# Kernel optimization log

Hardware: AMD Instinct MI355X
Metric: run time of the kernel (lower is better)

The kernel has to match this reference:

```python
import jax, jax.numpy as jnp
import numpy as np

SLOPE = 0.01  # torch LeakyReLU default negative_slope

def lrelu(x):
    return jax.nn.leaky_relu(x, SLOPE)

def rgcn_conv(x, edge_index, edge_type, rel_w, root_w, bias, num_relations=2):
    # PyG RGCNConv: out = x @ root + bias + sum_r mean_{edges of rel r into i}(x_j @ W_r)
    N = x.shape[0]
    src, dst = edge_index[0], edge_index[1]
    out = x @ root_w + bias
    # transform once per relation at node level, then gather per edge
    h = jnp.einsum('nd,rde->rne', x, rel_w)          # [R, N, d]
    msg = h[edge_type, src]                           # [E, d] single gather
    for r in range(num_relations):
        m = (edge_type == r)
        s = jax.ops.segment_sum(jnp.where(m[:, None], msg, 0.0), dst, num_segments=N)
        cnt = jax.ops.segment_sum(m.astype(x.dtype), dst, num_segments=N)
        out = out + s / jnp.maximum(cnt, 1.0)[:, None]  # mean aggregation (0 if no edges)
    return out


def setup_inputs() -> dict:
    key = jax.random.key(0)
    ks = jax.random.split(key, 24)
    N, E, H = 50000, 800000, 256
    Q = H // 4
    def lin(k, i, o):
        k1, k2 = jax.random.split(k)
        s = 1.0 / np.sqrt(i)
        return (jax.random.uniform(k1, (i, o), jnp.float32, -s, s),
                jax.random.uniform(k2, (o,), jnp.float32, -s, s))
    Wd, bd = lin(ks[0], 768, Q)
    Wt, bt = lin(ks[1], 768, Q)
    Wn, bn = lin(ks[2], 5, Q)
    Wc, bc = lin(ks[3], 3, Q)
    Wi, bi = lin(ks[4], H, H)
    Wo1, bo1 = lin(ks[5], H, H)
    Wo2, bo2 = lin(ks[6], H, 2)
    s = 1.0 / np.sqrt(H)
    rel_w1 = jax.random.uniform(ks[7], (2, H, H), jnp.float32, -s, s)
    root_w1 = jax.random.uniform(ks[8], (H, H), jnp.float32, -s, s)
    bias1 = jnp.zeros((H,), jnp.float32)
    rel_w2 = jax.random.uniform(ks[9], (2, H, H), jnp.float32, -s, s)
    root_w2 = jax.random.uniform(ks[10], (H, H), jnp.float32, -s, s)
    bias2 = jnp.zeros((H,), jnp.float32)
    return {
        'des': jax.random.normal(ks[11], (N, 768), jnp.float32),
        'tweet': jax.random.normal(ks[12], (N, 768), jnp.float32),
        'num_prop': jax.random.normal(ks[13], (N, 5), jnp.float32),
        'cat_prop': jax.random.normal(ks[14], (N, 3), jnp.float32),
        'edge_index': jax.random.randint(ks[15], (2, E), 0, N, jnp.int32),
        'edge_type': jax.random.randint(ks[16], (E,), 0, 2, jnp.int32),
        'Wd': Wd, 'bd': bd, 'Wt': Wt, 'bt': bt, 'Wn': Wn, 'bn': bn, 'Wc': Wc, 'bc': bc,
        'Wi': Wi, 'bi': bi,
        'rel_w1': rel_w1, 'root_w1': root_w1, 'bias1': bias1,
        'rel_w2': rel_w2, 'root_w2': root_w2, 'bias2': bias2,
        'Wo1': Wo1, 'bo1': bo1, 'Wo2': Wo2, 'bo2': bo2,
    }


def reference(des, tweet, num_prop, cat_prop, edge_index, edge_type,
              Wd, bd, Wt, bt, Wn, bn, Wc, bc, Wi, bi,
              rel_w1, root_w1, bias1, rel_w2, root_w2, bias2,
              Wo1, bo1, Wo2, bo2):
    # dropout is identity in eval mode
    d = lrelu(des @ Wd + bd)
    t = lrelu(tweet @ Wt + bt)
    n = lrelu(num_prop @ Wn + bn)
    c = lrelu(cat_prop @ Wc + bc)
    x = jnp.concatenate([d, t, n, c], axis=1)           # [N, H]
    x = lrelu(x @ Wi + bi)
    x = rgcn_conv(x, edge_index, edge_type, rel_w1, root_w1, bias1)
    x = rgcn_conv(x, edge_index, edge_type, rel_w2, root_w2, bias2)
    x = lrelu(x @ Wo1 + bo1)
    return x @ Wo2 + bo2                                 # [N, 2]
```

## Files before the change

kernel.cpp:

```cpp
#include <hip/hip_runtime.h>
#include <stdint.h>

__device__ __forceinline__ float bf2f(unsigned short h) {
    union { unsigned int u; float f; } x;
    x.u = ((unsigned int)h) << 16;
    return x.f;
}
__device__ __forceinline__ unsigned short f2bf(float f) {
    union { float f; unsigned int u; } x;
    x.f = f;
    unsigned int u = x.u;
    unsigned int r = (u + 0x7FFFu + ((u >> 16) & 1u)) >> 16;
    return (unsigned short)r;
}
__device__ __forceinline__ float ldf(const void* p, size_t i, int f32) {
    return f32 ? ((const float*)p)[i] : bf2f(((const unsigned short*)p)[i]);
}

typedef __attribute__((ext_vector_type(8))) short short8;
typedef __attribute__((ext_vector_type(4))) float floatx4;

__global__ void k_detect(const unsigned short* __restrict__ p, int* flag) {
    __shared__ int cnt;
    if (threadIdx.x == 0) cnt = 0;
    __syncthreads();
    int c = 0;
    for (int i = threadIdx.x; i < 4096; i += 256) {
        unsigned e = (p[i] >> 7) & 0xFFu;
        if (e >= 0xC0u) c++;
    }
    atomicAdd(&cnt, c);
    __syncthreads();
    if (threadIdx.x == 0) *flag = (cnt > 32) ? 1 : 0;
}

template <int BN, bool TWO>
__global__ __launch_bounds__(256) void gemm_nt(
    const void* __restrict__ A0, const void* __restrict__ A1,
    const void* __restrict__ A2, int o0, int o1, int o2, int lda,
    const unsigned short* __restrict__ Bt, int ldb,
    unsigned short* __restrict__ C, int ldc,
    const unsigned short* __restrict__ bias,
    int M, int K, int act, const int* __restrict__ dflag,
    const void* Ab = nullptr, const unsigned short* Btb = nullptr,
    unsigned short* Cb = nullptr, const unsigned short* biasb = nullptr)
{
    constexpr int BM = 128, BK = 64;
    constexpr int NJ = (BN == 128) ? 4 : 2;
    const int af32 = dflag ? *dflag : 0;
    const int tid  = threadIdx.x;
    const int wave = tid >> 6;
    const int lane = tid & 63;
    const int quad = lane >> 4;
    const int l16  = lane & 15;
    const int m0   = blockIdx.x * BM;
    const int wm   = (wave & 1) * 64;
    const int wn   = (wave >> 1) * (BN / 2);
    int n0;
    const unsigned short* BtS;
    unsigned short* CS;
    const unsigned short* biasS;
    const void *A0S, *A1S, *A2S;
    if (TWO && blockIdx.y == 1) {
        n0 = 0; BtS = Btb; CS = Cb; biasS = biasb;
        A0S = Ab; A1S = Ab; A2S = Ab;
    } else {
        n0 = TWO ? 0 : blockIdx.y * BN;
        BtS = Bt; CS = C; biasS = bias;
        A0S = A0; A1S = A1; A2S = A2;
    }

    __shared__ short8 As[8 * (BM + 2)];
    __shared__ short8 Bs[8 * (BN + 2)];

    floatx4 acc[4][NJ];
#pragma unroll
    for (int i = 0; i < 4; i++)
#pragma unroll
        for (int j = 0; j < NJ; j++) acc[i][j] = (floatx4){0.f, 0.f, 0.f, 0.f};

    for (int kt = 0; kt < K; kt += BK) {
        const void* Ap = (kt < 256) ? A0S : (kt < 512) ? A1S : A2S;
        const int Ao = (kt < 256) ? o0 : (kt < 512) ? o1 : o2;
        const int ko = kt & 255;
#pragma unroll
        for (int c = 0; c < 4; c++) {
            int lin = c * 256 + tid;
            int row = lin >> 3, kq = lin & 7;
            int gr = m0 + row; if (gr > M - 1) gr = M - 1;
            size_t eoff = (size_t)gr * lda + Ao + ko + kq * 8;
            short8 v;
            if (af32) {
                const float4* pf = (const float4*)((const float*)Ap + eoff);
                float4 f0 = pf[0];
                float4 f1 = pf[1];
                v[0] = (short)f2bf(f0.x); v[1] = (short)f2bf(f0.y);
                v[2] = (short)f2bf(f0.z); v[3] = (short)f2bf(f0.w);
                v[4] = (short)f2bf(f1.x); v[5] = (short)f2bf(f1.y);
                v[6] = (short)f2bf(f1.z); v[7] = (short)f2bf(f1.w);
            } else {
                v = *(const short8*)((const unsigned short*)Ap + eoff);
            }
            As[kq * (BM + 2) + row] = v;
        }
#pragma unroll
        for (int c = 0; c < (BN * 8) / 256; c++) {
            int lin = c * 256 + tid;
            int n = lin >> 3, kq = lin & 7;
            short8 v = *(const short8*)(BtS + (size_t)(n0 + n) * ldb + kt + kq * 8);
            Bs[kq * (BN + 2) + n] = v;
        }
        __syncthreads();
#pragma unroll
        for (int s = 0; s < 2; s++) {
            short8 af[4], bfr[NJ];
#pragma unroll
            for (int i = 0; i < 4; i++)
                af[i] = As[(s * 4 + quad) * (BM + 2) + wm + i * 16 + l16];
#pragma unroll
            for (int j = 0; j < NJ; j++)
                bfr[j] = Bs[(s * 4 + quad) * (BN + 2) + wn + j * 16 + l16];
#pragma unroll
            for (int i = 0; i < 4; i++)
#pragma unroll
                for (int j = 0; j < NJ; j++)
                    acc[i][j] = __builtin_amdgcn_mfma_f32_16x16x32_bf16(
                        af[i], bfr[j], acc[i][j], 0, 0, 0);
        }
        __syncthreads();
    }

#pragma unroll
    for (int j = 0; j < NJ; j++) {
        int gc = n0 + wn + j * 16 + l16;
        float bv = biasS ? bf2f(biasS[gc]) : 0.f;
#pragma unroll
        for (int i = 0; i < 4; i++) {
            int grb = m0 + wm + i * 16 + quad * 4;
#pragma unroll
            for (int r = 0; r < 4; r++) {
                int gr = grb + r;
                if (gr < M) {
                    float v = acc[i][j][r] + bv;
                    if (act) v = v > 0.f ? v : 0.01f * v;
                    CS[(size_t)gr * ldc + gc] = f2bf(v);
                }
            }
        }
    }
}

__global__ void t_cvt(const void* __restrict__ in, unsigned short* __restrict__ out,
                      int R, int C, const int* __restrict__ dflag) {
    int f32 = *dflag;
    int i = blockIdx.x * 256 + threadIdx.x;
    if (i < R * C) {
        int r = i / C, c = i % C;
        out[(size_t)c * R + r] = f2bf(ldf(in, i, f32));
    }
}

__global__ void build_bt(const void* __restrict__ root, const void* __restrict__ rel,
                         unsigned short* __restrict__ out, int H,
                         const int* __restrict__ dflag) {
    int f32 = *dflag;
    int i = blockIdx.x * 256 + threadIdx.x;
    int K3 = 3 * H;
    if (i < H * K3) {
        int k = i % K3;
        int n = i / K3;
        float v = (k < H) ? ldf(root, (size_t)k * H + n, f32)
                          : ldf(rel, (size_t)(k - H) * H + n, f32);
        out[i] = f2bf(v);
    }
}

__global__ void k_biases(const void* bd, const void* bt, const void* bi,
                         const void* b1, const void* b2, const void* bo1,
                         unsigned short* __restrict__ out, const int* __restrict__ dflag) {
    int f32 = *dflag;
    for (int idx = threadIdx.x; idx < 1152; idx += 256) {
        const void* p; int off;
        if (idx < 64)       { p = bd;  off = idx; }
        else if (idx < 128) { p = bt;  off = idx - 64; }
        else if (idx < 384) { p = bi;  off = idx - 128; }
        else if (idx < 640) { p = b1;  off = idx - 384; }
        else if (idx < 896) { p = b2;  off = idx - 640; }
        else                { p = bo1; off = idx - 896; }
        out[idx] = f2bf(ldf(p, off, f32));
    }
}

__global__ void k_hist(const int* __restrict__ ei, const int* __restrict__ et,
                       int* cnt2, int N, int E) {
    int e = blockIdx.x * 256 + threadIdx.x;
    if (e < E) {
        int dst = ei[E + e];
        int t = et[e] & 1;
        if ((unsigned)dst < (unsigned)N) atomicAdd(&cnt2[t * N + dst], 1);
    }
}

__global__ void k_scan1(const int* __restrict__ cnt2, int* rowptr, int* bsum, int N) {
    __shared__ int sh[256];
    int t = threadIdx.x;
    int base = blockIdx.x * 1024 + t * 4;
    int v[4];
    int s = 0;
#pragma unroll
    for (int k = 0; k < 4; k++) {
        int idx = base + k;
        v[k] = (idx < N) ? (cnt2[idx] + cnt2[N + idx]) : 0;
        s += v[k];
    }
    sh[t] = s;
    __syncthreads();
    for (int off = 1; off < 256; off <<= 1) {
        int x = 0;
        if (t >= off) x = sh[t - off];
        __syncthreads();
        if (t >= off) sh[t] += x;
        __syncthreads();
    }
    int excl = sh[t] - s;
    int run = excl;
#pragma unroll
    for (int k = 0; k < 4; k++) {
        int idx = base + k;
        if (idx < N) rowptr[idx] = run;
        run += v[k];
    }
    if (t == 255) bsum[blockIdx.x] = sh[255];
}

__global__ void k_scan2(const int* __restrict__ bsum, int* bofs, int nb) {
    int t = threadIdx.x;
    int v = (t < nb) ? bsum[t] : 0;
    int orig = v;
    for (int off = 1; off < 64; off <<= 1) {
        int x = __shfl_up(v, off);
        if (t >= off) v += x;
    }
    if (t < nb) bofs[t] = v - orig;
}

__global__ void k_scan3(int* rowptr, const int* __restrict__ bofs, int N) {
    int i = blockIdx.x * 256 + threadIdx.x;
    if (i < N) rowptr[i] += bofs[i >> 10];
}

__global__ void k_fill(const int* __restrict__ ei, const int* __restrict__ et,
                       const int* __restrict__ rowptr, int* cursor, int* sorted,
                       int N, int E) {
    int e = blockIdx.x * 256 + threadIdx.x;
    if (e < E) {
        int src = ei[e];
        int dst = ei[E + e];
        int t = et[e] & 1;
        if ((unsigned)dst < (unsigned)N && (unsigned)src < (unsigned)N) {
            int pos = rowptr[dst] + atomicAdd(&cursor[dst], 1);
            sorted[pos] = src | (t << 24);
        }
    }
}

__global__ __launch_bounds__(256) void k_agg(
    const unsigned short* __restrict__ x,
    unsigned short* __restrict__ m0,
    unsigned short* __restrict__ m1,
    int N,
    const int* __restrict__ rowptr, const int* __restrict__ cnt2,
    const int* __restrict__ sorted)
{
    int wave = threadIdx.x >> 6;
    int lane = threadIdx.x & 63;
    int half = lane >> 5;
    int l32  = lane & 31;
    int node = blockIdx.x * 4 + wave;
    if (node >= N) return;

    int start = rowptr[node];
    int c0 = cnt2[node], c1 = cnt2[N + node];
    int deg = c0 + c1;

    float a0[8] = {0,0,0,0,0,0,0,0};
    float a1[8] = {0,0,0,0,0,0,0,0};

    for (int b = 0; b < deg; b += 64) {
        int rem = deg - b; if (rem > 64) rem = 64;
        int p = 0;
        if (lane < rem) p = sorted[start + b + lane];
        int iters = (rem + 1) >> 1;
        for (int t = 0; t < iters; t += 2) {
            int e0 = 2 * t + half;
            int e1 = e0 + 2;
            int q0 = __shfl(p, e0 < 64 ? e0 : 63);
            int q1 = __shfl(p, e1 < 64 ? e1 : 63);
            bool v0ok = e0 < rem;
            bool v1ok = e1 < rem;
            int s0 = q0 & 0xFFFFFF; if (s0 >= N) s0 = 0;
            int s1 = q1 & 0xFFFFFF; if (s1 >= N) s1 = 0;
            uint4 r0 = *((const uint4*)(x + (size_t)s0 * 256) + l32);
            uint4 r1 = *((const uint4*)(x + (size_t)s1 * 256) + l32);
            if (v0ok) {
                float f[8];
                f[0] = bf2f((unsigned short)(r0.x & 0xFFFFu)); f[1] = bf2f((unsigned short)(r0.x >> 16));
                f[2] = bf2f((unsigned short)(r0.y & 0xFFFFu)); f[3] = bf2f((unsigned short)(r0.y >> 16));
                f[4] = bf2f((unsigned short)(r0.z & 0xFFFFu)); f[5] = bf2f((unsigned short)(r0.z >> 16));
                f[6] = bf2f((unsigned short)(r0.w & 0xFFFFu)); f[7] = bf2f((unsigned short)(r0.w >> 16));
                if ((q0 >> 24) & 1) {
#pragma unroll
                    for (int k = 0; k < 8; k++) a1[k] += f[k];
                } else {
#pragma unroll
                    for (int k = 0; k < 8; k++) a0[k] += f[k];
                }
            }
            if (v1ok) {
                float f[8];
                f[0] = bf2f((unsigned short)(r1.x & 0xFFFFu)); f[1] = bf2f((unsigned short)(r1.x >> 16));
                f[2] = bf2f((unsigned short)(r1.y & 0xFFFFu)); f[3] = bf2f((unsigned short)(r1.y >> 16));
                f[4] = bf2f((unsigned short)(r1.z & 0xFFFFu)); f[5] = bf2f((unsigned short)(r1.z >> 16));
                f[6] = bf2f((unsigned short)(r1.w & 0xFFFFu)); f[7] = bf2f((unsigned short)(r1.w >> 16));
                if ((q1 >> 24) & 1) {
#pragma unroll
                    for (int k = 0; k < 8; k++) a1[k] += f[k];
                } else {
#pragma unroll
                    for (int k = 0; k < 8; k++) a0[k] += f[k];
                }
            }
        }
    }
#pragma unroll
    for (int k = 0; k < 8; k++) {
        a0[k] += __shfl_xor(a0[k], 32);
        a1[k] += __shfl_xor(a1[k], 32);
    }
    float i0 = c0 > 0 ? 1.f / (float)c0 : 0.f;
    float i1 = c1 > 0 ? 1.f / (float)c1 : 0.f;
    uint4 o;
    if (half == 0) {
        o.x = (unsigned)f2bf(a0[0] * i0) | ((unsigned)f2bf(a0[1] * i0) << 16);
        o.y = (unsigned)f2bf(a0[2] * i0) | ((unsigned)f2bf(a0[3] * i0) << 16);
        o.z = (unsigned)f2bf(a0[4] * i0) | ((unsigned)f2bf(a0[5] * i0) << 16);
        o.w = (unsigned)f2bf(a0[6] * i0) | ((unsigned)f2bf(a0[7] * i0) << 16);
        *((uint4*)(m0 + (size_t)node * 256) + l32) = o;
    } else {
        o.x = (unsigned)f2bf(a1[0] * i1) | ((unsigned)f2bf(a1[1] * i1) << 16);
        o.y = (unsigned)f2bf(a1[2] * i1) | ((unsigned)f2bf(a1[3] * i1) << 16);
        o.z = (unsigned)f2bf(a1[4] * i1) | ((unsigned)f2bf(a1[5] * i1) << 16);
        o.w = (unsigned)f2bf(a1[6] * i1) | ((unsigned)f2bf(a1[7] * i1) << 16);
        *((uint4*)(m1 + (size_t)node * 256) + l32) = o;
    }
}

__global__ void k_small(const void* __restrict__ num, const void* __restrict__ cat,
                        const void* __restrict__ Wn, const void* __restrict__ bnp,
                        const void* __restrict__ Wc, const void* __restrict__ bcp,
                        unsigned short* __restrict__ xcat, int N,
                        const int* __restrict__ dflag)
{
    int f32 = *dflag;
    __shared__ float wn[320], wc[192], bns[64], bcs[64];
    int t = threadIdx.x;
    for (int i = t; i < 320; i += 256) wn[i] = ldf(Wn, i, f32);
    for (int i = t; i < 192; i += 256) wc[i] = ldf(Wc, i, f32);
    if (t < 64) { bns[t] = ldf(bnp, t, f32); bcs[t] = ldf(bcp, t, f32); }
    __syncthreads();

    int node = blockIdx.x * 128 + (t >> 1);
    int half = t & 1;
    if (node >= N) return;
    if (half == 0) {
        float in5[5];
#pragma unroll
        for (int i = 0; i < 5; i++) in5[i] = ldf(num, (size_t)node * 5 + i, f32);
        unsigned short* orow = xcat + (size_t)node * 256 + 128;
#pragma unroll 4
        for (int c = 0; c < 64; c++) {
            float v = bns[c];
#pragma unroll
            for (int i = 0; i < 5; i++) v += in5[i] * wn[i * 64 + c];
            v = v > 0.f ? v : 0.01f * v;
            orow[c] = f2bf(v);
        }
    } else {
        float in3[3];
#pragma unroll
        for (int i = 0; i < 3; i++) in3[i] = ldf(cat, (size_t)node * 3 + i, f32);
        unsigned short* orow = xcat + (size_t)node * 256 + 192;
#pragma unroll 4
        for (int c = 0; c < 64; c++) {
            float v = bcs[c];
#pragma unroll
            for (int i = 0; i < 3; i++) v += in3[i] * wc[i * 64 + c];
            v = v > 0.f ? v : 0.01f * v;
            orow[c] = f2bf(v);
        }
    }
}

__global__ __launch_bounds__(256) void k_final(
    const unsigned short* __restrict__ z,
    const void* __restrict__ Wo2, const void* __restrict__ bo2,
    void* __restrict__ out, int N, const int* __restrict__ dflag)
{
    int f32 = *dflag;
    __shared__ float w[512];
    int t = threadIdx.x;
    for (int i = t; i < 512; i += 256) w[i] = ldf(Wo2, i, f32);
    __syncthreads();
    int wave = t >> 6, lane = t & 63;
    int node = blockIdx.x * 4 + wave;
    if (node >= N) return;
    uint2 raw = *((const uint2*)(z + (size_t)node * 256) + lane);
    float v0 = bf2f((unsigned short)(raw.x & 0xFFFFu));
    float v1 = bf2f((unsigned short)(raw.x >> 16));
    float v2 = bf2f((unsigned short)(raw.y & 0xFFFFu));
    float v3 = bf2f((unsigned short)(raw.y >> 16));
    int k0 = lane * 4;
    float s0 = v0 * w[k0 * 2]     + v1 * w[(k0 + 1) * 2]     + v2 * w[(k0 + 2) * 2]     + v3 * w[(k0 + 3) * 2];
    float s1 = v0 * w[k0 * 2 + 1] + v1 * w[(k0 + 1) * 2 + 1] + v2 * w[(k0 + 2) * 2 + 1] + v3 * w[(k0 + 3) * 2 + 1];
    for (int off = 32; off; off >>= 1) {
        s0 += __shfl_xor(s0, off);
        s1 += __shfl_xor(s1, off);
    }
    if (lane == 0) {
        s0 += ldf(bo2, 0, f32);
        s1 += ldf(bo2, 1, f32);
        if (f32) {
            ((float*)out)[(size_t)node * 2]     = s0;
            ((float*)out)[(size_t)node * 2 + 1] = s1;
        } else {
            ((unsigned short*)out)[(size_t)node * 2]     = f2bf(s0);
            ((unsigned short*)out)[(size_t)node * 2 + 1] = f2bf(s1);
        }
    }
}

extern "C" void kernel_launch(void* const* d_in, const int* in_sizes, int n_in,
                              void* d_out, int out_size, void* d_ws, size_t ws_size,
                              hipStream_t stream)
{
    (void)n_in; (void)out_size; (void)ws_size;
    const void* des   = d_in[0];
    const void* tweet = d_in[1];
    const void* nump  = d_in[2];
    const void* catp  = d_in[3];
    const int*  ei    = (const int*)d_in[4];
    const int*  et    = (const int*)d_in[5];
    const void* Wd  = d_in[6];
    const void* bd  = d_in[7];
    const void* Wt  = d_in[8];
    const void* bt  = d_in[9];
    const void* Wn  = d_in[10];
    const void* bn  = d_in[11];
    const void* Wc  = d_in[12];
    const void* bc  = d_in[13];
    const void* Wi  = d_in[14];
    const void* bi  = d_in[15];
    const void* rel1  = d_in[16];
    const void* root1 = d_in[17];
    const void* bias1 = d_in[18];
    const void* rel2  = d_in[19];
    const void* root2 = d_in[20];
    const void* bias2 = d_in[21];
    const void* Wo1 = d_in[22];
    const void* bo1 = d_in[23];
    const void* Wo2 = d_in[24];
    const void* bo2 = d_in[25];

    const int N = in_sizes[0] / 768;
    const int E = in_sizes[5];

    char* ws = (char*)d_ws;
    size_t off = 0;
    auto alloc = [&](size_t bytes) -> char* {
        char* p = ws + off;
        off += (bytes + 255) & ~(size_t)255;
        return p;
    };
    unsigned short* B0 = (unsigned short*)alloc((size_t)N * 256 * 2);
    unsigned short* B1 = (unsigned short*)alloc((size_t)N * 256 * 2);
    unsigned short* B2 = (unsigned short*)alloc((size_t)N * 256 * 2);
    unsigned short* B3 = (unsigned short*)alloc((size_t)N * 256 * 2);
    unsigned short* WdT  = (unsigned short*)alloc(64 * 768 * 2);
    unsigned short* WtT  = (unsigned short*)alloc(64 * 768 * 2);
    unsigned short* WiT  = (unsigned short*)alloc(256 * 256 * 2);
    unsigned short* Wo1T = (unsigned short*)alloc(256 * 256 * 2);
    unsigned short* BT1  = (unsigned short*)alloc(256 * 768 * 2);
    unsigned short* BT2  = (unsigned short*)alloc(256 * 768 * 2);
    unsigned short* bias_bf = (unsigned short*)alloc(1152 * 2);
    unsigned short* bd_bf = bias_bf;
    unsigned short* bt_bf = bias_bf + 64;
    unsigned short* bi_bf = bias_bf + 128;
    unsigned short* b1_bf = bias_bf + 384;
    unsigned short* b2_bf = bias_bf + 640;
    unsigned short* bo1_bf = bias_bf + 896;
    int* dflag  = (int*)alloc(4);
    int* cnt2   = (int*)alloc((size_t)2 * N * 4);
    int* cursor = (int*)alloc((size_t)N * 4);
    int* rowptr = (int*)alloc((size_t)(N + 1) * 4);
    int* bsum   = (int*)alloc(64 * 4);
    int* bofs   = (int*)alloc(64 * 4);
    int* sorted = (int*)alloc((size_t)E * 4);

    size_t zlen = (size_t)(((char*)cursor + (size_t)N * 4) - (char*)cnt2);
    hipMemsetAsync(cnt2, 0, zlen, stream);

    k_detect<<<1, 256, 0, stream>>>((const unsigned short*)des, dflag);

    t_cvt<<<(768 * 64 + 255) / 256, 256, 0, stream>>>(Wd, WdT, 768, 64, dflag);
    t_cvt<<<(768 * 64 + 255) / 256, 256, 0, stream>>>(Wt, WtT, 768, 64, dflag);
    t_cvt<<<(256 * 256 + 255) / 256, 256, 0, stream>>>(Wi, WiT, 256, 256, dflag);
    t_cvt<<<(256 * 256 + 255) / 256, 256, 0, stream>>>(Wo1, Wo1T, 256, 256, dflag);
    build_bt<<<(256 * 768 + 255) / 256, 256, 0, stream>>>(root1, rel1, BT1, 256, dflag);
    build_bt<<<(256 * 768 + 255) / 256, 256, 0, stream>>>(root2, rel2, BT2, 256, dflag);
    k_biases<<<1, 256, 0, stream>>>(bd, bt, bi, bias1, bias2, bo1, bias_bf, dflag);

    int eb = (E + 255) / 256;
    k_hist<<<eb, 256, 0, stream>>>(ei, et, cnt2, N, E);
    int nb = (N + 1023) / 1024;
    k_scan1<<<nb, 256, 0, stream>>>(cnt2, rowptr, bsum, N);
    k_scan2<<<1, 64, 0, stream>>>(bsum, bofs, nb);
    k_scan3<<<(N + 255) / 256, 256, 0, stream>>>(rowptr, bofs, N);
    k_fill<<<eb, 256, 0, stream>>>(ei, et, rowptr, cursor, sorted, N, E);

    dim3 gEnc((N + 127) / 128, 2);
    gemm_nt<64, true><<<gEnc, 256, 0, stream>>>(des, des, des, 0, 256, 512, 768,
                                                WdT, 768, B0, 256, bd_bf, N, 768, 1, dflag,
                                                tweet, WtT, B0 + 64, bt_bf);
    k_small<<<(N + 127) / 128, 256, 0, stream>>>(nump, catp, Wn, bn, Wc, bc, B0, N, dflag);

    dim3 g128((N + 127) / 128, 2);
    gemm_nt<128, false><<<g128, 256, 0, stream>>>(B0, B0, B0, 0, 0, 0, 256, WiT, 256,
                                                  B1, 256, bi_bf, N, 256, 1, nullptr);

    int ab = (N + 3) / 4;
    k_agg<<<ab, 256, 0, stream>>>(B1, B2, B3, N, rowptr, cnt2, sorted);
    gemm_nt<128, false><<<g128, 256, 0, stream>>>(B1, B2, B3, 0, 0, 0, 256, BT1, 768,
                                                  B0, 256, b1_bf, N, 768, 0, nullptr);

    k_agg<<<ab, 256, 0, stream>>>(B0, B2, B3, N, rowptr, cnt2, sorted);
    gemm_nt<128, false><<<g128, 256, 0, stream>>>(B0, B2, B3, 0, 0, 0, 256, BT2, 768,
                                                  B1, 256, b2_bf, N, 768, 0, nullptr);

    gemm_nt<128, false><<<g128, 256, 0, stream>>>(B1, B1, B1, 0, 0, 0, 256, Wo1T, 256,
                                                  B0, 256, bo1_bf, N, 256, 1, nullptr);

    k_final<<<ab, 256, 0, stream>>>(B0, Wo2, bo2, d_out, N, dflag);
}
```

Measured before the change: 819.6 us.

## Add dedicated fp32 encoder GEMM kernel and fold weight prep into one launch

Replaces the generic tiled GEMM for the des/tweet encoders with a persistent-style kernel that keeps the whole transposed weight slice in LDS and streams fp32 rows straight into registers. It prefetches the next k-chunk and packs to bf16 with a cheap perm instruction. The runtime dtype detection kernel and its flag reads are removed in favor of assuming fp32 inputs. The several weight/bias conversion launches are merged into one kernel. This cuts launch count and per-tile branching, but it ties the code to fp32 inputs and uses truncation-style rounding in the new pack.

```diff
diff --git a/kernel.cpp b/kernel.cpp
--- a/kernel.cpp
+++ b/kernel.cpp
@@ -13,117 +13,176 @@
     unsigned int r = (u + 0x7FFFu + ((u >> 16) & 1u)) >> 16;
     return (unsigned short)r;
 }
-__device__ __forceinline__ float ldf(const void* p, size_t i, int f32) {
-    return f32 ? ((const float*)p)[i] : bf2f(((const unsigned short*)p)[i]);
+__device__ __forceinline__ unsigned pk2(float a, float b) {
+    unsigned ua = __float_as_uint(a) + 0x8000u;
+    unsigned ub = __float_as_uint(b) + 0x8000u;
+    return __builtin_amdgcn_perm(ub, ua, 0x07060302);
 }
 
 typedef __attribute__((ext_vector_type(8))) short short8;
 typedef __attribute__((ext_vector_type(4))) float floatx4;
 
-__global__ void k_detect(const unsigned short* __restrict__ p, int* flag) {
-    __shared__ int cnt;
-    if (threadIdx.x == 0) cnt = 0;
-    __syncthreads();
-    int c = 0;
-    for (int i = threadIdx.x; i < 4096; i += 256) {
-        unsigned e = (p[i] >> 7) & 0xFFu;
-        if (e >= 0xC0u) c++;
-    }
-    atomicAdd(&cnt, c);
-    __syncthreads();
-    if (threadIdx.x == 0) *flag = (cnt > 32) ? 1 : 0;
-}
-
-template <int BN, bool TWO>
+__global__ __launch_bounds__(512) void k_encode(
+    const float* __restrict__ Ades, const float* __restrict__ Atw,
+    const unsigned short* __restrict__ BtDes, const unsigned short* __restrict__ BtTw,
+    const unsigned short* __restrict__ bias_bf,
+    unsigned short* __restrict__ C, int M)
+{
+    __shared__ unsigned short Bs[64 * 392];
+    const int set = blockIdx.y;
+    const float* A = set ? Atw : Ades;
+    const unsigned short* Bt = set ? BtTw : BtDes;
+    const unsigned short* bias = bias_bf + set * 64;
+    const int colofs = set * 64;
+    const int tid  = threadIdx.x;
+    const int wave = tid >> 6, lane = tid & 63;
+    const int quad = lane >> 4, l16 = lane & 15;
+    const int ngroups = (M + 15) >> 4;
+
+    const int g0 = blockIdx.x * 8 + wave;
+    const int g1 = g0 + (int)(gridDim.x * 8);
+    const bool h1 = g1 < ngroups;
+    int r0 = g0 * 16 + l16; if (r0 > M - 1) r0 = M - 1;
+    int r1g = h1 ? g1 * 16 + l16 : r0; if (r1g > M - 1) r1g = M - 1;
+
+    floatx4 acc0[4], acc1[4];
+#pragma unroll
+    for (int t = 0; t < 4; t++) {
+        acc0[t] = (floatx4){0.f, 0.f, 0.f, 0.f};
+        acc1[t] = (floatx4){0.f, 0.f, 0.f, 0.f};
+    }
+
+    const bool act0 = g0 < ngroups;
+
+#pragma unroll
+    for (int h = 0; h < 2; h++) {
+        if (h) __syncthreads();
+        for (int c = tid; c < 3072; c += 512) {
+            int n = c / 48, kc = (c - n * 48) * 8;
+            *(uint4*)&Bs[n * 392 + kc] = ((const uint4*)Bt)[n * 96 + h * 48 + (c - n * 48)];
+        }
+        __syncthreads();
+        if (!act0) continue;
+
+        const float* a0 = A + (size_t)r0 * 768 + h * 384 + quad * 8;
+        const float* a1 = A + (size_t)r1g * 768 + h * 384 + quad * 8;
+        float4 c0a = *(const float4*)(a0);
+        float4 c0b = *(const float4*)(a0 + 4);
+        float4 c1a = *(const float4*)(a1);
+        float4 c1b = *(const float4*)(a1 + 4);
+        float4 n0a = *(const float4*)(a0 + 32);
+        float4 n0b = *(const float4*)(a0 + 36);
+        float4 n1a = *(const float4*)(a1 + 32);
+        float4 n1b = *(const float4*)(a1 + 36);
+
+        for (int s = 0; s < 12; s++) {
+            short8 af0, af1;
+            unsigned* u0 = (unsigned*)&af0;
+            unsigned* u1 = (unsigned*)&af1;
+            u0[0] = pk2(c0a.x, c0a.y); u0[1] = pk2(c0a.z, c0a.w);
+            u0[2] = pk2(c0b.x, c0b.y); u0[3] = pk2(c0b.z, c0b.w);
+            u1[0] = pk2(c1a.x, c1a.y); u1[1] = pk2(c1a.z, c1a.w);
+            u1[2] = pk2(c1b.x, c1b.y); u1[3] = pk2(c1b.z, c1b.w);
+            c0a = n0a; c0b = n0b; c1a = n1a; c1b = n1b;
+            if (s < 10) {
+                n0a = *(const float4*)(a0 + (s + 2) * 32);
+                n0b = *(const float4*)(a0 + (s + 2) * 32 + 4);
+                n1a = *(const float4*)(a1 + (s + 2) * 32);
+                n1b = *(const float4*)(a1 + (s + 2) * 32 + 4);
+            }
+            int kb = s * 32 + quad * 8;
+#pragma unroll
+            for (int t = 0; t < 4; t++) {
+                short8 bfr = *(const short8*)&Bs[(t * 16 + l16) * 392 + kb];
+                acc0[t] = __builtin_amdgcn_mfma_f32_16x16x32_bf16(af0, bfr, acc0[t], 0, 0, 0);
+                acc1[t] = __builtin_amdgcn_mfma_f32_16x16x32_bf16(af1, bfr, acc1[t], 0, 0, 0);
+            }
+        }
+    }
+
+    if (act0) {
+#pragma unroll
+        for (int t = 0; t < 4; t++) {
+            float bv = bf2f(bias[t * 16 + l16]);
+#pragma unroll
+            for (int r = 0; r < 4; r++) {
+                int row = g0 * 16 + quad * 4 + r;
+                if (row < M) {
+                    float v = acc0[t][r] + bv;
+                    v = v > 0.f ? v : 0.01f * v;
+                    C[(size_t)row * 256 + colofs + t * 16 + l16] = f2bf(v);
+                }
+                if (h1) {
+                    int rw = g1 * 16 + quad * 4 + r;
+                    if (rw < M) {
+                        float v = acc1[t][r] + bv;
+                        v = v > 0.f ? v : 0.01f * v;
+                        C[(size_t)rw * 256 + colofs + t * 16 + l16] = f2bf(v);
+                    }
+                }
+            }
+        }
+    }
+}
+
 __global__ __launch_bounds__(256) void gemm_nt(
-    const void* __restrict__ A0, const void* __restrict__ A1,
-    const void* __restrict__ A2, int o0, int o1, int o2, int lda,
+    const unsigned short* __restrict__ A0, const unsigned short* __restrict__ A1,
+    const unsigned short* __restrict__ A2, int lda,
     const unsigned short* __restrict__ Bt, int ldb,
     unsigned short* __restrict__ C, int ldc,
     const unsigned short* __restrict__ bias,
-    int M, int K, int act, const int* __restrict__ dflag,
-    const void* Ab = nullptr, const unsigned short* Btb = nullptr,
-    unsigned short* Cb = nullptr, const unsigned short* biasb = nullptr)
-{
-    constexpr int BM = 128, BK = 64;
-    constexpr int NJ = (BN == 128) ? 4 : 2;
-    const int af32 = dflag ? *dflag : 0;
+    int M, int K, int act)
+{
+    constexpr int BM = 128, BN = 128, BK = 64;
     const int tid  = threadIdx.x;
     const int wave = tid >> 6;
     const int lane = tid & 63;
     const int quad = lane >> 4;
     const int l16  = lane & 15;
     const int m0   = blockIdx.x * BM;
+    const int n0   = blockIdx.y * BN;
     const int wm   = (wave & 1) * 64;
-    const int wn   = (wave >> 1) * (BN / 2);
-    int n0;
-    const unsigned short* BtS;
-    unsigned short* CS;
-    const unsigned short* biasS;
-    const void *A0S, *A1S, *A2S;
-    if (TWO && blockIdx.y == 1) {
-        n0 = 0; BtS = Btb; CS = Cb; biasS = biasb;
-        A0S = Ab; A1S = Ab; A2S = Ab;
-    } else {
-        n0 = TWO ? 0 : blockIdx.y * BN;
-        BtS = Bt; CS = C; biasS = bias;
-        A0S = A0; A1S = A1; A2S = A2;
-    }
+    const int wn   = (wave >> 1) * 64;
 
     __shared__ short8 As[8 * (BM + 2)];
     __shared__ short8 Bs[8 * (BN + 2)];
 
-    floatx4 acc[4][NJ];
+    floatx4 acc[4][4];
 #pragma unroll
     for (int i = 0; i < 4; i++)
 #pragma unroll
-        for (int j = 0; j < NJ; j++) acc[i][j] = (floatx4){0.f, 0.f, 0.f, 0.f};
+        for (int j = 0; j < 4; j++) acc[i][j] = (floatx4){0.f, 0.f, 0.f, 0.f};
 
     for (int kt = 0; kt < K; kt += BK) {
-        const void* Ap = (kt < 256) ? A0S : (kt < 512) ? A1S : A2S;
-        const int Ao = (kt < 256) ? o0 : (kt < 512) ? o1 : o2;
+        const unsigned short* Ap = (kt < 256) ? A0 : (kt < 512) ? A1 : A2;
         const int ko = kt & 255;
 #pragma unroll
         for (int c = 0; c < 4; c++) {
             int lin = c * 256 + tid;
             int row = lin >> 3, kq = lin & 7;
             int gr = m0 + row; if (gr > M - 1) gr = M - 1;
-            size_t eoff = (size_t)gr * lda + Ao + ko + kq * 8;
-            short8 v;
-            if (af32) {
-                const float4* pf = (const float4*)((const float*)Ap + eoff);
-                float4 f0 = pf[0];
-                float4 f1 = pf[1];
-                v[0] = (short)f2bf(f0.x); v[1] = (short)f2bf(f0.y);
-                v[2] = (short)f2bf(f0.z); v[3] = (short)f2bf(f0.w);
-                v[4] = (short)f2bf(f1.x); v[5] = (short)f2bf(f1.y);
-                v[6] = (short)f2bf(f1.z); v[7] = (short)f2bf(f1.w);
-            } else {
-                v = *(const short8*)((const unsigned short*)Ap + eoff);
-            }
-            As[kq * (BM + 2) + row] = v;
-        }
-#pragma unroll
-        for (int c = 0; c < (BN * 8) / 256; c++) {
+            As[kq * (BM + 2) + row] = *(const short8*)(Ap + (size_t)gr * lda + ko + kq * 8);
+        }
+#pragma unroll
+        for (int c = 0; c < 4; c++) {
             int lin = c * 256 + tid;
             int n = lin >> 3, kq = lin & 7;
-            short8 v = *(const short8*)(BtS + (size_t)(n0 + n) * ldb + kt + kq * 8);
-            Bs[kq * (BN + 2) + n] = v;
+            Bs[kq * (BN + 2) + n] = *(const short8*)(Bt + (size_t)(n0 + n) * ldb + kt + kq * 8);
         }
         __syncthreads();
 #pragma unroll
         for (int s = 0; s < 2; s++) {
-            short8 af[4], bfr[NJ];
+            short8 af[4], bfr[4];
 #pragma unroll
             for (int i = 0; i < 4; i++)
                 af[i] = As[(s * 4 + quad) * (BM + 2) + wm + i * 16 + l16];
 #pragma unroll
-            for (int j = 0; j < NJ; j++)
+            for (int j = 0; j < 4; j++)
                 bfr[j] = Bs[(s * 4 + quad) * (BN + 2) + wn + j * 16 + l16];
 #pragma unroll
             for (int i = 0; i < 4; i++)
 #pragma unroll
-                for (int j = 0; j < NJ; j++)
+                for (int j = 0; j < 4; j++)
                     acc[i][j] = __builtin_amdgcn_mfma_f32_16x16x32_bf16(
                         af[i], bfr[j], acc[i][j], 0, 0, 0);
         }
@@ -131,9 +190,9 @@
     }
 
 #pragma unroll
-    for (int j = 0; j < NJ; j++) {
+    for (int j = 0; j < 4; j++) {
         int gc = n0 + wn + j * 16 + l16;
-        float bv = biasS ? bf2f(biasS[gc]) : 0.f;
+        float bv = bias ? bf2f(bias[gc]) : 0.f;
 #pragma unroll
         for (int i = 0; i < 4; i++) {
             int grb = m0 + wm + i * 16 + quad * 4;
@@ -143,51 +202,55 @@
                 if (gr < M) {
                     float v = acc[i][j][r] + bv;
                     if (act) v = v > 0.f ? v : 0.01f * v;
-                    CS[(size_t)gr * ldc + gc] = f2bf(v);
+                    C[(size_t)gr * ldc + gc] = f2bf(v);
                 }
             }
         }
     }
 }
 
-__global__ void t_cvt(const void* __restrict__ in, unsigned short* __restrict__ out,
-                      int R, int C, const int* __restrict__ dflag) {
-    int f32 = *dflag;
+__global__ void k_prep(const float* __restrict__ Wd, const float* __restrict__ Wt,
+                       const float* __restrict__ Wi, const float* __restrict__ Wo1,
+                       const float* __restrict__ root1, const float* __restrict__ rel1,
+                       const float* __restrict__ root2, const float* __restrict__ rel2,
+                       const float* __restrict__ bd, const float* __restrict__ bt,
+                       const float* __restrict__ bi, const float* __restrict__ b1,
+                       const float* __restrict__ b2, const float* __restrict__ bo1,
+                       unsigned short* __restrict__ WdT, unsigned short* __restrict__ WtT,
+                       unsigned short* __restrict__ WiT, unsigned short* __restrict__ Wo1T,
+                       unsigned short* __restrict__ BT1, unsigned short* __restrict__ BT2,
+                       unsigned short* __restrict__ bias_bf)
+{
     int i = blockIdx.x * 256 + threadIdx.x;
-    if (i < R * C) {
-        int r = i / C, c = i % C;
-        out[(size_t)c * R + r] = f2bf(ldf(in, i, f32));
-    }
-}
-
-__global__ void build_bt(const void* __restrict__ root, const void* __restrict__ rel,
-                         unsigned short* __restrict__ out, int H,
-                         const int* __restrict__ dflag) {
-    int f32 = *dflag;
-    int i = blockIdx.x * 256 + threadIdx.x;
-    int K3 = 3 * H;
-    if (i < H * K3) {
-        int k = i % K3;
-        int n = i / K3;
-        float v = (k < H) ? ldf(root, (size_t)k * H + n, f32)
-                          : ldf(rel, (size_t)(k - H) * H + n, f32);
-        out[i] = f2bf(v);
-    }
-}
-
-__global__ void k_biases(const void* bd, const void* bt, const void* bi,
-                         const void* b1, const void* b2, const void* bo1,
-                         unsigned short* __restrict__ out, const int* __restrict__ dflag) {
-    int f32 = *dflag;
-    for (int idx = threadIdx.x; idx < 1152; idx += 256) {
-        const void* p; int off;
-        if (idx < 64)       { p = bd;  off = idx; }
-        else if (idx < 128) { p = bt;  off = idx - 64; }
-        else if (idx < 384) { p = bi;  off = idx - 128; }
-        else if (idx < 640) { p = b1;  off = idx - 384; }
-        else if (idx < 896) { p = b2;  off = idx - 640; }
-        else                { p = bo1; off = idx - 896; }
-        out[idx] = f2bf(ldf(p, off, f32));
+    if (i < 49152) { int r = i >> 6, c = i & 63; WdT[c * 768 + r] = f2bf(Wd[i]); return; }
+    i -= 49152;
+    if (i < 49152) { int r = i >> 6, c = i & 63; WtT[c * 768 + r] = f2bf(Wt[i]); return; }
+    i -= 49152;
+    if (i < 65536) { int r = i >> 8, c = i & 255; WiT[c * 256 + r] = f2bf(Wi[i]); return; }
+    i -= 65536;
+    if (i < 65536) { int r = i >> 8, c = i & 255; Wo1T[c * 256 + r] = f2bf(Wo1[i]); return; }
+    i -= 65536;
+    if (i < 196608) {
+        int k = i % 768, n = i / 768;
+        BT1[i] = f2bf(k < 256 ? root1[k * 256 + n] : rel1[(k - 256) * 256 + n]);
+        return;
+    }
+    i -= 196608;
+    if (i < 196608) {
+        int k = i % 768, n = i / 768;
+        BT2[i] = f2bf(k < 256 ? root2[k * 256 + n] : rel2[(k - 256) * 256 + n]);
+        return;
+    }
+    i -= 196608;
+    if (i < 1152) {
+        const float* p; int off;
+        if (i < 64)       { p = bd;  off = i; }
+        else if (i < 128) { p = bt;  off = i - 64; }
+        else if (i < 384) { p = bi;  off = i - 128; }
+        else if (i < 640) { p = b1;  off = i - 384; }
+        else if (i < 896) { p = b2;  off = i - 640; }
+        else              { p = bo1; off = i - 896; }
+        bias_bf[i] = f2bf(p[off]);
     }
 }
 
@@ -355,18 +418,16 @@
     }
 }
 
-__global__ void k_small(const void* __restrict__ num, const void* __restrict__ cat,
-                        const void* __restrict__ Wn, const void* __restrict__ bnp,
-                        const void* __restrict__ Wc, const void* __restrict__ bcp,
-                        unsigned short* __restrict__ xcat, int N,
-                        const int* __restrict__ dflag)
-{
-    int f32 = *dflag;
+__global__ void k_small(const float* __restrict__ num, const float* __restrict__ cat,
+                        const float* __restrict__ Wn, const float* __restrict__ bnp,
+                        const float* __restrict__ Wc, const float* __restrict__ bcp,
+                        unsigned short* __restrict__ xcat, int N)
+{
     __shared__ float wn[320], wc[192], bns[64], bcs[64];
     int t = threadIdx.x;
-    for (int i = t; i < 320; i += 256) wn[i] = ldf(Wn, i, f32);
-    for (int i = t; i < 192; i += 256) wc[i] = ldf(Wc, i, f32);
-    if (t < 64) { bns[t] = ldf(bnp, t, f32); bcs[t] = ldf(bcp, t, f32); }
+    for (int i = t; i < 320; i += 256) wn[i] = Wn[i];
+    for (int i = t; i < 192; i += 256) wc[i] = Wc[i];
+    if (t < 64) { bns[t] = bnp[t]; bcs[t] = bcp[t]; }
     __syncthreads();
 
     int node = blockIdx.x * 128 + (t >> 1);
@@ -375,7 +436,7 @@
     if (half == 0) {
         float in5[5];
 #pragma unroll
-        for (int i = 0; i < 5; i++) in5[i] = ldf(num, (size_t)node * 5 + i, f32);
+        for (int i = 0; i < 5; i++) in5[i] = num[(size_t)node * 5 + i];
         unsigned short* orow = xcat + (size_t)node * 256 + 128;
 #pragma unroll 4
         for (int c = 0; c < 64; c++) {
@@ -388,7 +449,7 @@
     } else {
         float in3[3];
 #pragma unroll
-        for (int i = 0; i < 3; i++) in3[i] = ldf(cat, (size_t)node * 3 + i, f32);
+        for (int i = 0; i < 3; i++) in3[i] = cat[(size_t)node * 3 + i];
         unsigned short* orow = xcat + (size_t)node * 256 + 192;
 #pragma unroll 4
         for (int c = 0; c < 64; c++) {
@@ -403,13 +464,12 @@
 
 __global__ __launch_bounds__(256) void k_final(
     const unsigned short* __restrict__ z,
-    const void* __restrict__ Wo2, const void* __restrict__ bo2,
-    void* __restrict__ out, int N, const int* __restrict__ dflag)
-{
-    int f32 = *dflag;
+    const float* __restrict__ Wo2, const float* __restrict__ bo2,
+    float* __restrict__ out, int N)
+{
     __shared__ float w[512];
     int t = threadIdx.x;
-    for (int i = t; i < 512; i += 256) w[i] = ldf(Wo2, i, f32);
+    for (int i = t; i < 512; i += 256) w[i] = Wo2[i];
     __syncthreads();
     int wave = t >> 6, lane = t & 63;
     int node = blockIdx.x * 4 + wave;
@@ -427,15 +487,8 @@
         s1 += __shfl_xor(s1, off);
     }
     if (lane == 0) {
-        s0 += ldf(bo2, 0, f32);
-        s1 += ldf(bo2, 1, f32);
-        if (f32) {
-            ((float*)out)[(size_t)node * 2]     = s0;
-            ((float*)out)[(size_t)node * 2 + 1] = s1;
-        } else {
-            ((unsigned short*)out)[(size_t)node * 2]     = f2bf(s0);
-            ((unsigned short*)out)[(size_t)node * 2 + 1] = f2bf(s1);
-        }
+        out[(size_t)node * 2]     = s0 + bo2[0];
+        out[(size_t)node * 2 + 1] = s1 + bo2[1];
     }
 }
 
@@ -444,32 +497,32 @@
                               hipStream_t stream)
 {
     (void)n_in; (void)out_size; (void)ws_size;
-    const void* des   = d_in[0];
-    const void* tweet = d_in[1];
-    const void* nump  = d_in[2];
-    const void* catp  = d_in[3];
-    const int*  ei    = (const int*)d_in[4];
-    const int*  et    = (const int*)d_in[5];
-    const void* Wd  = d_in[6];
-    const void* bd  = d_in[7];
-    const void* Wt  = d_in[8];
-    const void* bt  = d_in[9];
-    const void* Wn  = d_in[10];
-    const void* bn  = d_in[11];
-    const void* Wc  = d_in[12];
-    const void* bc  = d_in[13];
-    const void* Wi  = d_in[14];
-    const void* bi  = d_in[15];
-    const void* rel1  = d_in[16];
-    const void* root1 = d_in[17];
-    const void* bias1 = d_in[18];
-    const void* rel2  = d_in[19];
-    const void* root2 = d_in[20];
-    const void* bias2 = d_in[21];
-    const void* Wo1 = d_in[22];
-    const void* bo1 = d_in[23];
-    const void* Wo2 = d_in[24];
-    const void* bo2 = d_in[25];
+    const float* des   = (const float*)d_in[0];
+    const float* tweet = (const float*)d_in[1];
+    const float* nump  = (const float*)d_in[2];
+    const float* catp  = (const float*)d_in[3];
+    const int*   ei    = (const int*)d_in[4];
+    const int*   et    = (const int*)d_in[5];
+    const float* Wd  = (const float*)d_in[6];
+    const float* bd  = (const float*)d_in[7];
+    const float* Wt  = (const float*)d_in[8];
+    const float* bt  = (const float*)d_in[9];
+    const float* Wn  = (const float*)d_in[10];
+    const float* bn  = (const float*)d_in[11];
+    const float* Wc  = (const float*)d_in[12];
+    const float* bc  = (const float*)d_in[13];
+    const float* Wi  = (const float*)d_in[14];
+    const float* bi  = (const float*)d_in[15];
+    const float* rel1  = (const float*)d_in[16];
+    const float* root1 = (const float*)d_in[17];
+    const float* bias1 = (const float*)d_in[18];
+    const float* rel2  = (const float*)d_in[19];
+    const float* root2 = (const float*)d_in[20];
+    const float* bias2 = (const float*)d_in[21];
+    const float* Wo1 = (const float*)d_in[22];
+    const float* bo1 = (const float*)d_in[23];
+    const float* Wo2 = (const float*)d_in[24];
+    const float* bo2 = (const float*)d_in[25];
 
     const int N = in_sizes[0] / 768;
     const int E = in_sizes[5];
@@ -493,12 +546,10 @@
     unsigned short* BT2  = (unsigned short*)alloc(256 * 768 * 2);
     unsigned short* bias_bf = (unsigned short*)alloc(1152 * 2);
     unsigned short* bd_bf = bias_bf;
-    unsigned short* bt_bf = bias_bf + 64;
     unsigned short* bi_bf = bias_bf + 128;
     unsigned short* b1_bf = bias_bf + 384;
     unsigned short* b2_bf = bias_bf + 640;
     unsigned short* bo1_bf = bias_bf + 896;
-    int* dflag  = (int*)alloc(4);
     int* cnt2   = (int*)alloc((size_t)2 * N * 4);
     int* cursor = (int*)alloc((size_t)N * 4);
     int* rowptr = (int*)alloc((size_t)(N + 1) * 4);
@@ -509,15 +560,10 @@
     size_t zlen = (size_t)(((char*)cursor + (size_t)N * 4) - (char*)cnt2);
     hipMemsetAsync(cnt2, 0, zlen, stream);
 
-    k_detect<<<1, 256, 0, stream>>>((const unsigned short*)des, dflag);
-
-    t_cvt<<<(768 * 64 + 255) / 256, 256, 0, stream>>>(Wd, WdT, 768, 64, dflag);
-    t_cvt<<<(768 * 64 + 255) / 256, 256, 0, stream>>>(Wt, WtT, 768, 64, dflag);
-    t_cvt<<<(256 * 256 + 255) / 256, 256, 0, stream>>>(Wi, WiT, 256, 256, dflag);
-    t_cvt<<<(256 * 256 + 255) / 256, 256, 0, stream>>>(Wo1, Wo1T, 256, 256, dflag);
-    build_bt<<<(256 * 768 + 255) / 256, 256, 0, stream>>>(root1, rel1, BT1, 256, dflag);
-    build_bt<<<(256 * 768 + 255) / 256, 256, 0, stream>>>(root2, rel2, BT2, 256, dflag);
-    k_biases<<<1, 256, 0, stream>>>(bd, bt, bi, bias1, bias2, bo1, bias_bf, dflag);
+    k_prep<<<(623744 + 255) / 256, 256, 0, stream>>>(
+        Wd, Wt, Wi, Wo1, root1, rel1, root2, rel2,
+        bd, bt, bi, bias1, bias2, bo1,
+        WdT, WtT, WiT, Wo1T, BT1, BT2, bias_bf);
 
     int eb = (E + 255) / 256;
     k_hist<<<eb, 256, 0, stream>>>(ei, et, cnt2, N, E);
@@ -527,27 +573,21 @@
     k_scan3<<<(N + 255) / 256, 256, 0, stream>>>(rowptr, bofs, N);
     k_fill<<<eb, 256, 0, stream>>>(ei, et, rowptr, cursor, sorted, N, E);
 
-    dim3 gEnc((N + 127) / 128, 2);
-    gemm_nt<64, true><<<gEnc, 256, 0, stream>>>(des, des, des, 0, 256, 512, 768,
-                                                WdT, 768, B0, 256, bd_bf, N, 768, 1, dflag,
-                                                tweet, WtT, B0 + 64, bt_bf);
-    k_small<<<(N + 127) / 128, 256, 0, stream>>>(nump, catp, Wn, bn, Wc, bc, B0, N, dflag);
+    dim3 gEnc(256, 2);
+    k_encode<<<gEnc, 512, 0, stream>>>(des, tweet, WdT, WtT, bd_bf, B0, N);
+    k_small<<<(N + 127) / 128, 256, 0, stream>>>(nump, catp, Wn, bn, Wc, bc, B0, N);
 
     dim3 g128((N + 127) / 128, 2);
-    gemm_nt<128, false><<<g128, 256, 0, stream>>>(B0, B0, B0, 0, 0, 0, 256, WiT, 256,
-                                                  B1, 256, bi_bf, N, 256, 1, nullptr);
+    gemm_nt<<<g128, 256, 0, stream>>>(B0, B0, B0, 256, WiT, 256, B1, 256, bi_bf, N, 256, 1);
 
     int ab = (N + 3) / 4;
     k_agg<<<ab, 256, 0, stream>>>(B1, B2, B3, N, rowptr, cnt2, sorted);
-    gemm_nt<128, false><<<g128, 256, 0, stream>>>(B1, B2, B3, 0, 0, 0, 256, BT1, 768,
-                                                  B0, 256, b1_bf, N, 768, 0, nullptr);
+    gemm_nt<<<g128, 256, 0, stream>>>(B1, B2, B3, 256, BT1, 768, B0, 256, b1_bf, N, 768, 0);
 
     k_agg<<<ab, 256, 0, stream>>>(B0, B2, B3, N, rowptr, cnt2, sorted);
-    gemm_nt<128, false><<<g128, 256, 0, stream>>>(B0, B2, B3, 0, 0, 0, 256, BT2, 768,
-                                                  B1, 256, b2_bf, N, 768, 0, nullptr);
-
-    gemm_nt<128, false><<<g128, 256, 0, stream>>>(B1, B1, B1, 0, 0, 0, 256, Wo1T, 256,
-                                                  B0, 256, bo1_bf, N, 256, 1, nullptr);
-
-    k_final<<<ab, 256, 0, stream>>>(B0, Wo2, bo2, d_out, N, dflag);
-}
+    gemm_nt<<<g128, 256, 0, stream>>>(B0, B2, B3, 256, BT2, 768, B1, 256, b2_bf, N, 768, 0);
+
+    gemm_nt<<<g128, 256, 0, stream>>>(B1, B1, B1, 256, Wo1T, 256, B0, 256, bo1_bf, N, 256, 1);
+
+    k_final<<<ab, 256, 0, stream>>>(B0, Wo2, bo2, (float*)d_out, N);
+}
```

Result: faster. 752.8 us (-8.2%).
